# Kernel tuning notes

Hardware: AMD Instinct MI355X
Metric: run time of the kernel (lower is better)

## Reference

```python
import jax, jax.numpy as jnp
import numpy as np

NUM_HEADS = 28
HEAD_DIM = 128
NUM_KV_HEADS = 4
N_REP = NUM_HEADS // NUM_KV_HEADS  # 7
ROPE_THETA = 1000000.0
CUR_IND = 0  # prefill into empty cache
_K_MASK = float(jnp.finfo(jnp.bfloat16).min)


def _rope_sincos(position_ids, head_dim, theta):
    # position_ids: (B, T) int -> sin, cos: (B, T, head_dim//2)
    half = head_dim // 2
    fraction = jnp.arange(half, dtype=jnp.float32) / half
    timescale = theta ** fraction  # (half,)
    ang = position_ids[..., None].astype(jnp.float32) / timescale
    return jnp.sin(ang), jnp.cos(ang)


def _apply_rope(x, sin, cos):
    # x: (B, T, N, H); sin/cos: (B, T, H//2)
    half = x.shape[-1] // 2
    x1, x2 = x[..., :half], x[..., half:]
    s, c = sin[:, :, None, :], cos[:, :, None, :]
    return jnp.concatenate([x1 * c - x2 * s, x2 * c + x1 * s], axis=-1).astype(x.dtype)


def setup_inputs() -> dict:
    key = jax.random.key(0)
    ks = jax.random.split(key, 8)
    B, T, D = 2, 1024, 3584
    KVD = NUM_KV_HEADS * HEAD_DIM  # 512
    sd = 1.0 / np.sqrt(D)
    return {
        "x": jax.random.normal(ks[0], (B, T, D), jnp.float32),
        "segment_ids": jnp.ones((B, T), jnp.int32),
        "k_cache": jnp.zeros((B, T, NUM_KV_HEADS, HEAD_DIM), jnp.float32),
        "v_cache": jnp.zeros((B, T, NUM_KV_HEADS, HEAD_DIM), jnp.float32),
        "Wq": jax.random.normal(ks[1], (D, D), jnp.float32) * sd,
        "bq": jax.random.normal(ks[2], (D,), jnp.float32) * 0.01,
        "Wk": jax.random.normal(ks[3], (D, KVD), jnp.float32) * sd,
        "bk": jax.random.normal(ks[4], (KVD,), jnp.float32) * 0.01,
        "Wv": jax.random.normal(ks[5], (D, KVD), jnp.float32) * sd,
        "bv": jax.random.normal(ks[6], (KVD,), jnp.float32) * 0.01,
        "Wo": jax.random.normal(ks[7], (D, D), jnp.float32) * sd,
    }


def reference(x, segment_ids, k_cache, v_cache, Wq, bq, Wk, bk, Wv, bv, Wo):
    b, t, _ = x.shape
    cache_size = k_cache.shape[1]
    scale = HEAD_DIM ** -0.5

    q = (x @ Wq + bq).reshape(b, t, NUM_HEADS, HEAD_DIM)
    k = (x @ Wk + bk).reshape(b, t, NUM_KV_HEADS, HEAD_DIM)
    v = (x @ Wv + bv).reshape(b, t, NUM_KV_HEADS, HEAD_DIM)

    # left pads and positions (cache.start_ind initialized <0 -> becomes left_pads)
    valid = segment_ids != 0
    left_pads = jnp.sum(jnp.cumsum(valid, axis=-1) == 0, axis=-1).astype(jnp.int32)  # (B,)
    start_ind = left_pads
    position_ids = (jnp.cumsum(valid, axis=-1) - 1).astype(jnp.int32) + CUR_IND  # (B, T)

    sin, cos = _rope_sincos(position_ids, HEAD_DIM, ROPE_THETA)
    q = _apply_rope(q, sin, cos)
    k = _apply_rope(k, sin, cos)

    # write into KV cache at cur_ind (prefill: overwrites [0:t])
    k_cache = jax.lax.dynamic_update_slice(k_cache, k, (0, CUR_IND, 0, 0))
    v_cache = jax.lax.dynamic_update_slice(v_cache, v, (0, CUR_IND, 0, 0))

    q_gqa = q.reshape(b, t, NUM_KV_HEADS, N_REP, HEAD_DIM)
    attn_logits = jnp.einsum('BTKGH,BSKH->BTSKG', q_gqa, k_cache) * scale

    q_pos = CUR_IND + jnp.arange(t, dtype=jnp.int32)[None, :] - start_ind[:, None]  # (B,T)
    ts = jnp.arange(cache_size, dtype=jnp.int32)
    kv_segment_ids = (ts[None, :] >= start_ind[:, None]) & (ts[None, :] < CUR_IND + t)  # (B,S)
    k_pos = ts[None, :] - start_ind[:, None]  # (B,S)
    causal_mask = k_pos[:, None, :] <= q_pos[:, :, None]          # (B,T,S)
    segment_mask = kv_segment_ids[:, None, :] == segment_ids[:, :, None]  # (B,T,S)
    final_mask = (causal_mask & segment_mask)[:, :, :, None, None]  # (B,T,S,1,1)

    attn_logits = jnp.where(final_mask, attn_logits, _K_MASK)
    attn_weights = jax.nn.softmax(attn_logits.astype(jnp.float32), axis=2).astype(attn_logits.dtype)

    qkv = jnp.einsum('BTSKG,BSKH->BTKGH', attn_weights, v_cache)
    qkv = qkv.reshape(b, t, NUM_HEADS * HEAD_DIM)
    return qkv @ Wo
```

## Files before the change

kernel.cpp:

```cpp
#include <hip/hip_runtime.h>
#include <hip/hip_bf16.h>
#include <stdint.h>

#define T_SEQ 1024
#define DMODEL 3584
#define KVDIM 512
#define NQH 28
#define NKVH 4
#define NREP 7
#define HD 128
#define NTOT 4608
#define BATCH 2
#define MROWS 2048
#define KMASK (-3.3895314e38f)

typedef __attribute__((ext_vector_type(8))) short short8;
typedef __attribute__((ext_vector_type(4))) float f32x4;

__device__ __forceinline__ short8 ld_s8(const __hip_bfloat16* p) {
    return *reinterpret_cast<const short8*>(p);
}

__device__ __forceinline__ f32x4 mfma16(short8 a, short8 b, f32x4 c) {
    return __builtin_amdgcn_mfma_f32_16x16x32_bf16(a, b, c, 0, 0, 0);
}

__device__ __forceinline__ void gload_lds16(const __hip_bfloat16* g, __hip_bfloat16* l) {
    __builtin_amdgcn_global_load_lds(
        (const __attribute__((address_space(1))) unsigned int*)g,
        (__attribute__((address_space(3))) unsigned int*)l,
        16, 0, 0);
}

__global__ void scan_kernel(const int* __restrict__ seg, int* __restrict__ pos_ids,
                            int* __restrict__ left_pads) {
    int b = blockIdx.x;
    int t = threadIdx.x;
    __shared__ int cum[T_SEQ];
    __shared__ int lp;
    if (t == 0) lp = 0;
    cum[t] = (seg[b * T_SEQ + t] != 0) ? 1 : 0;
    __syncthreads();
    for (int off = 1; off < T_SEQ; off <<= 1) {
        int add = (t >= off) ? cum[t - off] : 0;
        __syncthreads();
        cum[t] += add;
        __syncthreads();
    }
    pos_ids[b * T_SEQ + t] = cum[t] - 1;
    if (cum[t] == 0) atomicAdd(&lp, 1);
    __syncthreads();
    if (t == 0) left_pads[b] = lp;
}

__global__ void convert_bf16(const float* __restrict__ x, __hip_bfloat16* __restrict__ xb, int n) {
    int i = (blockIdx.x * blockDim.x + threadIdx.x) * 4;
    if (i >= n) return;
    float4 v = *reinterpret_cast<const float4*>(x + i);
    union { __hip_bfloat16 h[4]; uint2 u; } o;
    o.h[0] = __float2bfloat16(v.x);
    o.h[1] = __float2bfloat16(v.y);
    o.h[2] = __float2bfloat16(v.z);
    o.h[3] = __float2bfloat16(v.w);
    *reinterpret_cast<uint2*>(xb + i) = o.u;
}

__global__ void transpose_convert(const float* __restrict__ W, __hip_bfloat16* __restrict__ WT,
                                  int K, int N) {
    __shared__ float tile[32][33];
    int n0 = blockIdx.x * 32, k0 = blockIdx.y * 32;
    int tx = threadIdx.x, ty = threadIdx.y;
#pragma unroll
    for (int j = 0; j < 4; j++)
        tile[ty + j * 8][tx] = W[(size_t)(k0 + ty + j * 8) * N + n0 + tx];
    __syncthreads();
#pragma unroll
    for (int j = 0; j < 4; j++)
        WT[(size_t)(n0 + ty + j * 8) * K + k0 + tx] = __float2bfloat16(tile[tx][ty + j * 8]);
}

__global__ void transpose_v(const __hip_bfloat16* __restrict__ qkv, __hip_bfloat16* __restrict__ vbT) {
    __shared__ __hip_bfloat16 tile[32][33];
    int c0 = blockIdx.x * 32;
    int s0 = blockIdx.y * 32;
    int b = blockIdx.z;
    int tx = threadIdx.x, ty = threadIdx.y;
#pragma unroll
    for (int j = 0; j < 4; j++)
        tile[ty + j * 8][tx] = qkv[(size_t)(b * T_SEQ + s0 + ty + j * 8) * NTOT + DMODEL + KVDIM + c0 + tx];
    __syncthreads();
#pragma unroll
    for (int j = 0; j < 4; j++)
        vbT[((size_t)b * KVDIM + c0 + ty + j * 8) * T_SEQ + s0 + tx] = tile[tx][ty + j * 8];
}

__global__ void rope_kernel(__hip_bfloat16* __restrict__ qkv, const int* __restrict__ pos_ids) {
    int row = blockIdx.x;
    int tid = threadIdx.x;
    __shared__ float sc[2][64];
    float fpos = (float)pos_ids[row];
    if (tid < 64) {
        float freq = exp2f((float)tid * (-0.31143076632024816f));
        float ang = fpos * freq;
        sc[0][tid] = sinf(ang);
        sc[1][tid] = cosf(ang);
    }
    __syncthreads();
    __hip_bfloat16* rp = qkv + (size_t)row * NTOT;
    for (int p = tid; p < 32 * 64; p += 256) {
        int hh = p >> 6;
        int j = p & 63;
        int cb = (hh < NQH) ? hh * HD : DMODEL + (hh - NQH) * HD;
        float s = sc[0][j], c = sc[1][j];
        float x1 = __bfloat162float(rp[cb + j]);
        float x2 = __bfloat162float(rp[cb + j + 64]);
        rp[cb + j] = __float2bfloat16(x1 * c - x2 * s);
        rp[cb + j + 64] = __float2bfloat16(x2 * c + x1 * s);
    }
}

template <int MODE>
__global__ __launch_bounds__(256, 2) void gemm_bt(
    const __hip_bfloat16* __restrict__ A, const __hip_bfloat16* __restrict__ BT,
    int M, int N, int K,
    const float* __restrict__ bq, const float* __restrict__ bk, const float* __restrict__ bv,
    __hip_bfloat16* __restrict__ Cb, float* __restrict__ Cf) {
    __shared__ __hip_bfloat16 As[128 * 32];
    __shared__ __hip_bfloat16 Bs[128 * 32];
    int tid = threadIdx.x;
    int w = tid >> 6, lane = tid & 63;
    int wr = w >> 1, wc = w & 1;
    int bm = blockIdx.y * 128, bn = blockIdx.x * 128;
    int r16 = lane & 15, g4 = lane >> 4;
    int lrow = lane >> 2;
    int lk = (lane & 3) * 8;
    int c0 = w * 2, c1 = w * 2 + 1;

    const __hip_bfloat16* Ag0 = A + (size_t)(bm + c0 * 16 + lrow) * K + lk;
    const __hip_bfloat16* Ag1 = A + (size_t)(bm + c1 * 16 + lrow) * K + lk;
    const __hip_bfloat16* Bg0 = BT + (size_t)(bn + c0 * 16 + lrow) * K + lk;
    const __hip_bfloat16* Bg1 = BT + (size_t)(bn + c1 * 16 + lrow) * K + lk;
    __hip_bfloat16* Al0 = As + c0 * 512;
    __hip_bfloat16* Al1 = As + c1 * 512;
    __hip_bfloat16* Bl0 = Bs + c0 * 512;
    __hip_bfloat16* Bl1 = Bs + c1 * 512;

    f32x4 acc[4][4] = {};
    for (int kt = 0; kt < K; kt += 32) {
        gload_lds16(Ag0 + kt, Al0);
        gload_lds16(Ag1 + kt, Al1);
        gload_lds16(Bg0 + kt, Bl0);
        gload_lds16(Bg1 + kt, Bl1);
        __syncthreads();
        short8 aF[4], bF[4];
#pragma unroll
        for (int m = 0; m < 4; m++)
            aF[m] = *reinterpret_cast<const short8*>(As + (wr * 64 + m * 16 + r16) * 32 + g4 * 8);
#pragma unroll
        for (int n = 0; n < 4; n++)
            bF[n] = *reinterpret_cast<const short8*>(Bs + (wc * 64 + n * 16 + r16) * 32 + g4 * 8);
#pragma unroll
        for (int m = 0; m < 4; m++)
#pragma unroll
            for (int n = 0; n < 4; n++)
                acc[m][n] = mfma16(aF[m], bF[n], acc[m][n]);
        __syncthreads();
    }
#pragma unroll
    for (int m = 0; m < 4; m++) {
#pragma unroll
        for (int n = 0; n < 4; n++) {
            int row0 = bm + wr * 64 + m * 16 + g4 * 4;
            int col = bn + wc * 64 + n * 16 + r16;
            float badd = 0.0f;
            if (MODE == 0)
                badd = (col < DMODEL) ? bq[col]
                       : (col < DMODEL + KVDIM ? bk[col - DMODEL] : bv[col - DMODEL - KVDIM]);
#pragma unroll
            for (int reg = 0; reg < 4; reg++) {
                float v = acc[m][n][reg] + badd;
                if (MODE == 0)
                    Cb[(size_t)(row0 + reg) * N + col] = __float2bfloat16(v);
                else
                    Cf[(size_t)(row0 + reg) * N + col] = v;
            }
        }
    }
}

__global__ __launch_bounds__(448, 4) void attn_kernel(
    const __hip_bfloat16* __restrict__ qkv, const __hip_bfloat16* __restrict__ vbT,
    const int* __restrict__ seg, const int* __restrict__ left_pads,
    __hip_bfloat16* __restrict__ attn_out) {
    int qt_raw = blockIdx.x;
    int kvh = blockIdx.y;
    int b = blockIdx.z;
    int qt = (b == 1) ? 63 - qt_raw : qt_raw;
    int tid = threadIdx.x;
    int w = tid >> 6;
    int lane = tid & 63;
    int r = lane & 15, g = lane >> 4;
    int h = kvh * NREP + w;
    int start = left_pads[b];
    const float scale = 0.08838834764831845f;

    __shared__ __hip_bfloat16 Kt[2][64 * 128];
    __shared__ __hip_bfloat16 Vt[2][128 * 64];
    __shared__ __hip_bfloat16 Ps[NREP][16 * 64];

    const __hip_bfloat16* Qp = qkv + (size_t)(b * T_SEQ + qt * 16 + r) * NTOT + h * HD;
    short8 qf[4];
#pragma unroll
    for (int kc = 0; kc < 4; kc++) qf[kc] = ld_s8(Qp + kc * 32 + g * 8);

    int qrow = qt * 16 + r;
    int segq = seg[b * T_SEQ + qrow];
    int qpos = qrow - start;

    float m_run = -__builtin_inff();
    float l_part = 0.0f;
    f32x4 acc[8] = {};

    const __hip_bfloat16* Kg = qkv + (size_t)(b * T_SEQ) * NTOT + DMODEL + kvh * HD;
    const __hip_bfloat16* Vg = vbT + ((size_t)b * KVDIM + kvh * HD) * T_SEQ;
    int nt = qt / 4 + 1;

    auto stage = [&](int buf, int t) {
        int s0 = t * 64;
        for (int i = w; i < 16; i += NREP) {
            int slot = i * 64 + lane;
            int row = slot >> 4;
            int c = ((slot & 15) << 4) ^ ((row & 7) << 4);
            gload_lds16(Kg + (size_t)(s0 + row) * NTOT + (c >> 1), &Kt[buf][i * 512]);
        }
        for (int i = w; i < 16; i += NREP) {
            int slot = i * 64 + lane;
            int d = slot >> 3;
            int c = ((slot & 7) << 4) ^ ((d & 7) << 4);
            gload_lds16(Vg + (size_t)d * T_SEQ + s0 + (c >> 1), &Vt[buf][i * 512]);
        }
    };

    stage(0, 0);
    __syncthreads();
    int buf = 0;
    for (int t = 0; t < nt; t++) {
        if (t + 1 < nt) stage(buf ^ 1, t + 1);
        int s0 = t * 64;
        f32x4 sacc[4] = {};
#pragma unroll
        for (int n = 0; n < 4; n++) {
#pragma unroll
            for (int kc = 0; kc < 4; kc++) {
                int col = (kc * 32 + g * 8) ^ ((r & 7) << 3);
                short8 kf = ld_s8(&Kt[buf][(n * 16 + r) * 128 + col]);
                sacc[n] = mfma16(kf, qf[kc], sacc[n]);
            }
        }
        float p[16];
        float mt = -__builtin_inff();
#pragma unroll
        for (int n = 0; n < 4; n++)
#pragma unroll
            for (int reg = 0; reg < 4; reg++) {
                int kv = s0 + n * 16 + g * 4 + reg;
                float val = sacc[n][reg] * scale;
                bool ok = (kv - start <= qpos) && (((kv >= start) ? 1 : 0) == segq);
                val = ok ? val : KMASK;
                p[n * 4 + reg] = val;
                mt = fmaxf(mt, val);
            }
        mt = fmaxf(mt, __shfl_xor(mt, 16, 64));
        mt = fmaxf(mt, __shfl_xor(mt, 32, 64));
        if (!__all(mt <= m_run + 8.0f)) {
            float mn = fmaxf(m_run, mt);
            float fac = __expf(m_run - mn);
            m_run = mn;
            l_part *= fac;
            float facr[4];
#pragma unroll
            for (int reg = 0; reg < 4; reg++) facr[reg] = __shfl(fac, g * 4 + reg, 64);
#pragma unroll
            for (int h7 = 0; h7 < 8; h7++)
#pragma unroll
                for (int reg = 0; reg < 4; reg++)
                    acc[h7][reg] *= facr[reg];
        }
#pragma unroll
        for (int i = 0; i < 16; i++) {
            p[i] = __expf(p[i] - m_run);
            l_part += p[i];
        }
#pragma unroll
        for (int n = 0; n < 4; n++) {
            union { __hip_bfloat16 h[4]; uint2 u; } pk;
#pragma unroll
            for (int reg = 0; reg < 4; reg++) pk.h[reg] = __float2bfloat16(p[n * 4 + reg]);
            int col = (n * 16 + g * 4) ^ ((r & 7) << 3);
            *reinterpret_cast<uint2*>(&Ps[w][r * 64 + col]) = pk.u;
        }
#pragma unroll
        for (int kc = 0; kc < 2; kc++) {
            int colp = (kc * 32 + g * 8) ^ ((r & 7) << 3);
            short8 a_pv = ld_s8(&Ps[w][r * 64 + colp]);
#pragma unroll
            for (int h7 = 0; h7 < 8; h7++) {
                int d = h7 * 16 + r;
                int colv = (kc * 32 + g * 8) ^ ((r & 7) << 3);
                short8 vf = ld_s8(&Vt[buf][d * 64 + colv]);
                acc[h7] = mfma16(a_pv, vf, acc[h7]);
            }
        }
        __syncthreads();
        buf ^= 1;
    }
    l_part += __shfl_xor(l_part, 16, 64);
    l_part += __shfl_xor(l_part, 32, 64);
    float invl[4];
#pragma unroll
    for (int reg = 0; reg < 4; reg++) invl[reg] = 1.0f / __shfl(l_part, g * 4 + reg, 64);
#pragma unroll
    for (int h7 = 0; h7 < 8; h7++)
#pragma unroll
        for (int reg = 0; reg < 4; reg++)
            attn_out[(size_t)(b * T_SEQ + qt * 16 + g * 4 + reg) * DMODEL + h * HD + h7 * 16 + r] =
                __float2bfloat16(acc[h7][reg] * invl[reg]);
}

extern "C" void kernel_launch(void* const* d_in, const int* in_sizes, int n_in,
                              void* d_out, int out_size, void* d_ws, size_t ws_size,
                              hipStream_t stream) {
    const float* x = (const float*)d_in[0];
    const int* seg = (const int*)d_in[1];
    const float* Wq = (const float*)d_in[4];
    const float* bq = (const float*)d_in[5];
    const float* Wk = (const float*)d_in[6];
    const float* bk = (const float*)d_in[7];
    const float* Wv = (const float*)d_in[8];
    const float* bv = (const float*)d_in[9];
    const float* Wo = (const float*)d_in[10];
    float* out = (float*)d_out;

    uint8_t* ws = (uint8_t*)d_ws;
    size_t off = 0;
    auto alloc = [&](size_t bytes) -> void* {
        void* p = ws + off;
        off += (bytes + 255) & ~(size_t)255;
        return p;
    };
    int* pos_ids = (int*)alloc(MROWS * sizeof(int));
    int* left_pads = (int*)alloc(16 * sizeof(int));
    __hip_bfloat16* xb = (__hip_bfloat16*)alloc((size_t)MROWS * DMODEL * 2);
    __hip_bfloat16* WqkvT = (__hip_bfloat16*)alloc((size_t)NTOT * DMODEL * 2);
    __hip_bfloat16* WoT = (__hip_bfloat16*)alloc((size_t)DMODEL * DMODEL * 2);
    __hip_bfloat16* qkv = (__hip_bfloat16*)alloc((size_t)MROWS * NTOT * 2);
    __hip_bfloat16* vbT = (__hip_bfloat16*)alloc((size_t)BATCH * KVDIM * T_SEQ * 2);
    __hip_bfloat16* attn = (__hip_bfloat16*)alloc((size_t)MROWS * DMODEL * 2);

    scan_kernel<<<BATCH, T_SEQ, 0, stream>>>(seg, pos_ids, left_pads);
    convert_bf16<<<(MROWS * DMODEL / 4 + 255) / 256, 256, 0, stream>>>(x, xb, MROWS * DMODEL);
    transpose_convert<<<dim3(DMODEL / 32, DMODEL / 32), dim3(32, 8), 0, stream>>>(Wq, WqkvT, DMODEL, DMODEL);
    transpose_convert<<<dim3(KVDIM / 32, DMODEL / 32), dim3(32, 8), 0, stream>>>(
        Wk, WqkvT + (size_t)DMODEL * DMODEL, DMODEL, KVDIM);
    transpose_convert<<<dim3(KVDIM / 32, DMODEL / 32), dim3(32, 8), 0, stream>>>(
        Wv, WqkvT + (size_t)(DMODEL + KVDIM) * DMODEL, DMODEL, KVDIM);
    transpose_convert<<<dim3(DMODEL / 32, DMODEL / 32), dim3(32, 8), 0, stream>>>(Wo, WoT, DMODEL, DMODEL);
    gemm_bt<0><<<dim3(NTOT / 128, MROWS / 128), 256, 0, stream>>>(
        xb, WqkvT, MROWS, NTOT, DMODEL, bq, bk, bv, qkv, nullptr);
    rope_kernel<<<MROWS, 256, 0, stream>>>(qkv, pos_ids);
    transpose_v<<<dim3(KVDIM / 32, T_SEQ / 32, BATCH), dim3(32, 8), 0, stream>>>(qkv, vbT);
    attn_kernel<<<dim3(T_SEQ / 16, NKVH, BATCH), 448, 0, stream>>>(qkv, vbT, seg, left_pads, attn);
    gemm_bt<1><<<dim3(DMODEL / 128, MROWS / 128), 256, 0, stream>>>(
        attn, WoT, MROWS, DMODEL, DMODEL, nullptr, nullptr, nullptr, nullptr, out);
}
```

Measured before the change: 425.1 us.

## Replace GEMM with 256x256 double-buffered, swizzled LDS tile kernel

Replaces the 128x128, K=32 single-buffered GEMM with a 256x256 tile, K=64, 512-thread kernel. It double-buffers LDS through direct global-to-LDS loads, XOR-swizzles the LDS layout to avoid bank conflicts, and interleaves prefetch of the next tile with MFMA phases using s_setprio. It also remaps block indices so neighbouring blocks share operand tiles in L2. The aim is to cut global traffic per FLOP and hide load latency. The cost is a large shared-memory footprint (128KB per block, which limits occupancy) and few blocks for the Wo GEMM (14x8=112), so some CUs may sit idle.

```diff
diff --git a/kernel.cpp b/kernel.cpp
--- a/kernel.cpp
+++ b/kernel.cpp
@@ -17,6 +17,9 @@
 typedef __attribute__((ext_vector_type(8))) short short8;
 typedef __attribute__((ext_vector_type(4))) float f32x4;
 
+#define SB()       asm volatile("s_barrier" ::: "memory")
+#define WAIT_VM0() asm volatile("s_waitcnt vmcnt(0)" ::: "memory")
+
 __device__ __forceinline__ short8 ld_s8(const __hip_bfloat16* p) {
     return *reinterpret_cast<const short8*>(p);
 }
@@ -120,57 +123,135 @@
 }
 
 template <int MODE>
-__global__ __launch_bounds__(256, 2) void gemm_bt(
+__global__ __launch_bounds__(512, 2) void gemm256(
     const __hip_bfloat16* __restrict__ A, const __hip_bfloat16* __restrict__ BT,
-    int M, int N, int K,
+    int M, int N, int K, int nbx,
     const float* __restrict__ bq, const float* __restrict__ bk, const float* __restrict__ bv,
     __hip_bfloat16* __restrict__ Cb, float* __restrict__ Cf) {
-    __shared__ __hip_bfloat16 As[128 * 32];
-    __shared__ __hip_bfloat16 Bs[128 * 32];
+    __shared__ __hip_bfloat16 As[2][256 * 64];
+    __shared__ __hip_bfloat16 Bs[2][256 * 64];
     int tid = threadIdx.x;
-    int w = tid >> 6, lane = tid & 63;
-    int wr = w >> 1, wc = w & 1;
-    int bm = blockIdx.y * 128, bn = blockIdx.x * 128;
+    int wv = tid >> 6, lane = tid & 63;
+    int wr = wv >> 2, wc = wv & 3;
     int r16 = lane & 15, g4 = lane >> 4;
-    int lrow = lane >> 2;
-    int lk = (lane & 3) * 8;
-    int c0 = w * 2, c1 = w * 2 + 1;
-
-    const __hip_bfloat16* Ag0 = A + (size_t)(bm + c0 * 16 + lrow) * K + lk;
-    const __hip_bfloat16* Ag1 = A + (size_t)(bm + c1 * 16 + lrow) * K + lk;
-    const __hip_bfloat16* Bg0 = BT + (size_t)(bn + c0 * 16 + lrow) * K + lk;
-    const __hip_bfloat16* Bg1 = BT + (size_t)(bn + c1 * 16 + lrow) * K + lk;
-    __hip_bfloat16* Al0 = As + c0 * 512;
-    __hip_bfloat16* Al1 = As + c1 * 512;
-    __hip_bfloat16* Bl0 = Bs + c0 * 512;
-    __hip_bfloat16* Bl1 = Bs + c1 * 512;
-
-    f32x4 acc[4][4] = {};
-    for (int kt = 0; kt < K; kt += 32) {
-        gload_lds16(Ag0 + kt, Al0);
-        gload_lds16(Ag1 + kt, Al1);
-        gload_lds16(Bg0 + kt, Bl0);
-        gload_lds16(Bg1 + kt, Bl1);
-        __syncthreads();
-        short8 aF[4], bF[4];
-#pragma unroll
-        for (int m = 0; m < 4; m++)
-            aF[m] = *reinterpret_cast<const short8*>(As + (wr * 64 + m * 16 + r16) * 32 + g4 * 8);
-#pragma unroll
-        for (int n = 0; n < 4; n++)
-            bF[n] = *reinterpret_cast<const short8*>(Bs + (wc * 64 + n * 16 + r16) * 32 + g4 * 8);
-#pragma unroll
-        for (int m = 0; m < 4; m++)
-#pragma unroll
-            for (int n = 0; n < 4; n++)
-                acc[m][n] = mfma16(aF[m], bF[n], acc[m][n]);
-        __syncthreads();
-    }
-#pragma unroll
-    for (int m = 0; m < 4; m++) {
+    int nwg = gridDim.x;
+    int sb = ((int)blockIdx.x & 7) * (nwg >> 3) + ((int)blockIdx.x >> 3);
+    int bx = sb % nbx, by = sb / nbx;
+    int bm = by * 256, bn = bx * 256;
+    int nt = K >> 6;
+
+    int lrow = lane >> 3;
+    int srcoff = ((lane & 7) * 8) ^ (lrow * 8);
+
+    auto stageA = [&](int buf, int t) {
+        const __hip_bfloat16* src = A + (size_t)t * 64 + srcoff;
+#pragma unroll
+        for (int h = 0; h < 2; h++)
+#pragma unroll
+            for (int i = 0; i < 2; i++) {
+                int r0 = h * 128 + wv * 16 + i * 8;
+                gload_lds16(src + (size_t)(bm + r0 + lrow) * K, &As[buf][r0 * 64]);
+            }
+    };
+    auto stageB = [&](int buf, int t) {
+        const __hip_bfloat16* src = BT + (size_t)t * 64 + srcoff;
+#pragma unroll
+        for (int h = 0; h < 2; h++)
+#pragma unroll
+            for (int i = 0; i < 2; i++) {
+                int r0 = h * 128 + wv * 16 + i * 8;
+                gload_lds16(src + (size_t)(bn + r0 + lrow) * K, &Bs[buf][r0 * 64]);
+            }
+    };
+    int swz = (r16 & 7) << 3;
+
+    f32x4 acc[8][4] = {};
+    stageA(0, 0);
+    stageB(0, 0);
+
+    for (int w = 0; w < nt; w++) {
+        int buf = w & 1;
+        WAIT_VM0();
+        SB();
+        short8 aF[4][2], bF0[2][2], bF1[2][2];
+#pragma unroll
+        for (int mi = 0; mi < 4; mi++)
+#pragma unroll
+            for (int ks = 0; ks < 2; ks++) {
+                int row = wr * 128 + mi * 16 + r16;
+                aF[mi][ks] = ld_s8(&As[buf][row * 64 + ((ks * 32 + g4 * 8) ^ swz)]);
+            }
+#pragma unroll
+        for (int ni = 0; ni < 2; ni++)
+#pragma unroll
+            for (int ks = 0; ks < 2; ks++) {
+                int row = wc * 64 + ni * 16 + r16;
+                bF0[ni][ks] = ld_s8(&Bs[buf][row * 64 + ((ks * 32 + g4 * 8) ^ swz)]);
+            }
+        if (w + 1 < nt) stageA(buf ^ 1, w + 1);
+        SB();
+        __builtin_amdgcn_s_setprio(1);
+#pragma unroll
+        for (int mi = 0; mi < 4; mi++)
+#pragma unroll
+            for (int ni = 0; ni < 2; ni++) {
+                acc[mi][ni] = mfma16(aF[mi][0], bF0[ni][0], acc[mi][ni]);
+                acc[mi][ni] = mfma16(aF[mi][1], bF0[ni][1], acc[mi][ni]);
+            }
+        __builtin_amdgcn_s_setprio(0);
+        SB();
+#pragma unroll
+        for (int ni = 0; ni < 2; ni++)
+#pragma unroll
+            for (int ks = 0; ks < 2; ks++) {
+                int row = wc * 64 + (2 + ni) * 16 + r16;
+                bF1[ni][ks] = ld_s8(&Bs[buf][row * 64 + ((ks * 32 + g4 * 8) ^ swz)]);
+            }
+        if (w + 1 < nt) stageB(buf ^ 1, w + 1);
+        SB();
+        __builtin_amdgcn_s_setprio(1);
+#pragma unroll
+        for (int mi = 0; mi < 4; mi++)
+#pragma unroll
+            for (int ni = 0; ni < 2; ni++) {
+                acc[mi][2 + ni] = mfma16(aF[mi][0], bF1[ni][0], acc[mi][2 + ni]);
+                acc[mi][2 + ni] = mfma16(aF[mi][1], bF1[ni][1], acc[mi][2 + ni]);
+            }
+        __builtin_amdgcn_s_setprio(0);
+        SB();
+#pragma unroll
+        for (int mi = 0; mi < 4; mi++)
+#pragma unroll
+            for (int ks = 0; ks < 2; ks++) {
+                int row = wr * 128 + 64 + mi * 16 + r16;
+                aF[mi][ks] = ld_s8(&As[buf][row * 64 + ((ks * 32 + g4 * 8) ^ swz)]);
+            }
+        SB();
+        __builtin_amdgcn_s_setprio(1);
+#pragma unroll
+        for (int mi = 0; mi < 4; mi++)
+#pragma unroll
+            for (int ni = 0; ni < 2; ni++) {
+                acc[4 + mi][ni] = mfma16(aF[mi][0], bF0[ni][0], acc[4 + mi][ni]);
+                acc[4 + mi][ni] = mfma16(aF[mi][1], bF0[ni][1], acc[4 + mi][ni]);
+            }
+        __builtin_amdgcn_s_setprio(0);
+        SB();
+        __builtin_amdgcn_s_setprio(1);
+#pragma unroll
+        for (int mi = 0; mi < 4; mi++)
+#pragma unroll
+            for (int ni = 0; ni < 2; ni++) {
+                acc[4 + mi][2 + ni] = mfma16(aF[mi][0], bF1[ni][0], acc[4 + mi][2 + ni]);
+                acc[4 + mi][2 + ni] = mfma16(aF[mi][1], bF1[ni][1], acc[4 + mi][2 + ni]);
+            }
+        __builtin_amdgcn_s_setprio(0);
+    }
+#pragma unroll
+    for (int m = 0; m < 8; m++) {
 #pragma unroll
         for (int n = 0; n < 4; n++) {
-            int row0 = bm + wr * 64 + m * 16 + g4 * 4;
+            int row0 = bm + wr * 128 + m * 16 + g4 * 4;
             int col = bn + wc * 64 + n * 16 + r16;
             float badd = 0.0f;
             if (MODE == 0)
@@ -365,11 +446,11 @@
     transpose_convert<<<dim3(KVDIM / 32, DMODEL / 32), dim3(32, 8), 0, stream>>>(
         Wv, WqkvT + (size_t)(DMODEL + KVDIM) * DMODEL, DMODEL, KVDIM);
     transpose_convert<<<dim3(DMODEL / 32, DMODEL / 32), dim3(32, 8), 0, stream>>>(Wo, WoT, DMODEL, DMODEL);
-    gemm_bt<0><<<dim3(NTOT / 128, MROWS / 128), 256, 0, stream>>>(
-        xb, WqkvT, MROWS, NTOT, DMODEL, bq, bk, bv, qkv, nullptr);
+    gemm256<0><<<dim3((NTOT / 256) * (MROWS / 256)), 512, 0, stream>>>(
+        xb, WqkvT, MROWS, NTOT, DMODEL, NTOT / 256, bq, bk, bv, qkv, nullptr);
     rope_kernel<<<MROWS, 256, 0, stream>>>(qkv, pos_ids);
     transpose_v<<<dim3(KVDIM / 32, T_SEQ / 32, BATCH), dim3(32, 8), 0, stream>>>(qkv, vbT);
     attn_kernel<<<dim3(T_SEQ / 16, NKVH, BATCH), 448, 0, stream>>>(qkv, vbT, seg, left_pads, attn);
-    gemm_bt<1><<<dim3(DMODEL / 128, MROWS / 128), 256, 0, stream>>>(
-        attn, WoT, MROWS, DMODEL, DMODEL, nullptr, nullptr, nullptr, nullptr, out);
-}
+    gemm256<1><<<dim3((DMODEL / 256) * (MROWS / 256)), 512, 0, stream>>>(
+        attn, WoT, MROWS, DMODEL, DMODEL, DMODEL / 256, nullptr, nullptr, nullptr, nullptr, out);
+}
```

Result: slower. 469.7 us (+10.5%).
